# Optimization experiments

Hardware: AMD Instinct MI355X
Metric: run time of the kernel (lower is better)

The kernel has to match this reference:

```python
import jax, jax.numpy as jnp
import numpy as np

D = 128          # embed_dim
T = 500000       # num tokens
N = 100000       # num nodes
EPS = 1e-5       # BatchNorm eps (torch default)


def _mlp(x, g, b, m, v, W1, b1, W2, b2):
    # _GTSMLP in eval mode: BatchNorm1d -> Linear -> ReLU -> Linear (dropouts are identity)
    h = (x - m) * jax.lax.rsqrt(v + EPS) * g + b
    h = jax.nn.relu(h @ W1.T + b1)
    return h @ W2.T + b2


def setup_inputs() -> dict:
    key = jax.random.key(0)
    ks = jax.random.split(key, 12)
    s = 0.02
    return {
        "x": jax.random.normal(ks[0], (T, D), jnp.float32),
        "node_features": jax.random.normal(ks[1], (N, D), jnp.float32),
        "node_batch": jax.random.randint(ks[2], (N,), 0, 8, jnp.int64),
        "token_index": jax.random.randint(ks[3], (2, T), 0, N, jnp.int64),
        # out_proj: BN(D) -> Linear(D, 2D) -> ReLU -> Linear(2D, 2D)
        "op_bn_g": jnp.ones((D,), jnp.float32),
        "op_bn_b": jnp.zeros((D,), jnp.float32),
        "op_bn_m": jnp.zeros((D,), jnp.float32),
        "op_bn_v": jnp.ones((D,), jnp.float32),
        "op_w1": jax.random.normal(ks[4], (2 * D, D), jnp.float32) * s,
        "op_b1": jnp.zeros((2 * D,), jnp.float32),
        "op_w2": jax.random.normal(ks[5], (2 * D, 2 * D), jnp.float32) * s,
        "op_b2": jnp.zeros((2 * D,), jnp.float32),
        # node_mlp: BN(D) -> Linear(D, D) -> ReLU -> Linear(D, D)
        "nm_bn_g": jnp.ones((D,), jnp.float32),
        "nm_bn_b": jnp.zeros((D,), jnp.float32),
        "nm_bn_m": jnp.zeros((D,), jnp.float32),
        "nm_bn_v": jnp.ones((D,), jnp.float32),
        "nm_w1": jax.random.normal(ks[6], (D, D), jnp.float32) * s,
        "nm_b1": jnp.zeros((D,), jnp.float32),
        "nm_w2": jax.random.normal(ks[7], (D, D), jnp.float32) * s,
        "nm_b2": jnp.zeros((D,), jnp.float32),
    }


def reference(x, node_features, node_batch, token_index,
              op_bn_g, op_bn_b, op_bn_m, op_bn_v, op_w1, op_b1, op_w2, op_b2,
              nm_bn_g, nm_bn_b, nm_bn_m, nm_bn_v, nm_w1, nm_b1, nm_w2, nm_b2):
    dim_size = node_batch.shape[0]
    y = _mlp(x, op_bn_g, op_bn_b, op_bn_m, op_bn_v, op_w1, op_b1, op_w2, op_b2)  # [T, 2D]
    # node_features is zeroed in the original; accumulate two scatter-sums
    nf = (jax.ops.segment_sum(y[:, :D], token_index[0], num_segments=dim_size)
          + jax.ops.segment_sum(y[:, D:], token_index[1], num_segments=dim_size))  # [N, D]
    return _mlp(nf, nm_bn_g, nm_bn_b, nm_bn_m, nm_bn_v, nm_w1, nm_b1, nm_w2, nm_b2)
```

## Files before the change

kernel.cpp:

```cpp
#include <hip/hip_runtime.h>
#include <hip/hip_bf16.h>

typedef __bf16 bf16_t;
typedef bf16_t bf16x8 __attribute__((ext_vector_type(8)));
typedef bf16_t bf16x4 __attribute__((ext_vector_type(4)));
typedef bf16_t bf16x2 __attribute__((ext_vector_type(2)));
typedef float  f32x4  __attribute__((ext_vector_type(4)));

#define EPS 1e-5f

__global__ __launch_bounds__(256) void prep_kernel(
    const float* __restrict__ op_w1, const float* __restrict__ op_w2,
    const float* __restrict__ nm_w1, const float* __restrict__ nm_w2,
    const float* __restrict__ op_g, const float* __restrict__ op_b,
    const float* __restrict__ op_m, const float* __restrict__ op_v,
    const float* __restrict__ nm_g, const float* __restrict__ nm_b,
    const float* __restrict__ nm_m, const float* __restrict__ nm_v,
    bf16_t* __restrict__ w1f, bf16_t* __restrict__ w2f,
    bf16_t* __restrict__ nw1f, bf16_t* __restrict__ nw2f,
    float* __restrict__ opsc, float* __restrict__ opsh,
    float* __restrict__ nmsc, float* __restrict__ nmsh)
{
    int t = blockIdx.x * 256 + threadIdx.x;
    if (t < 4096) {
        int g = t, lane = g & 63, nt = (g >> 6) & 15, kt = g >> 10;
        int n = nt * 16 + (lane & 15);
        int k0 = kt * 32 + (lane >> 4) * 8;
        const float* src = op_w1 + (size_t)n * 128 + k0;
        bf16x8 v;
        for (int j = 0; j < 8; ++j) v[j] = (bf16_t)src[j];
        *(bf16x8*)(w1f + (size_t)g * 8) = v;
    } else if (t < 12288) {
        int g = t - 4096, lane = g & 63, nt = (g >> 6) & 15, kt = g >> 10;
        int n = nt * 16 + (lane & 15);
        int k0 = kt * 32 + (lane >> 4) * 8;
        const float* src = op_w2 + (size_t)n * 256 + k0;
        bf16x8 v;
        for (int j = 0; j < 8; ++j) v[j] = (bf16_t)src[j];
        *(bf16x8*)(w2f + (size_t)g * 8) = v;
    } else if (t < 14336) {
        int g = t - 12288, lane = g & 63, nt = (g >> 6) & 7, kt = g >> 9;
        int n = nt * 16 + (lane & 15);
        int k0 = kt * 32 + (lane >> 4) * 8;
        const float* src = nm_w1 + (size_t)n * 128 + k0;
        bf16x8 v;
        for (int j = 0; j < 8; ++j) v[j] = (bf16_t)src[j];
        *(bf16x8*)(nw1f + (size_t)g * 8) = v;
    } else if (t < 16384) {
        int g = t - 14336, lane = g & 63, nt = (g >> 6) & 7, kt = g >> 9;
        int n = nt * 16 + (lane & 15);
        int k0 = kt * 32 + (lane >> 4) * 8;
        const float* src = nm_w2 + (size_t)n * 128 + k0;
        bf16x8 v;
        for (int j = 0; j < 8; ++j) v[j] = (bf16_t)src[j];
        *(bf16x8*)(nw2f + (size_t)g * 8) = v;
    } else if (t < 16512) {
        int c = t - 16384;
        float s = op_g[c] / sqrtf(op_v[c] + EPS);
        opsc[c] = s;
        opsh[c] = op_b[c] - op_m[c] * s;
    } else if (t < 16640) {
        int c = t - 16512;
        float s = nm_g[c] / sqrtf(nm_v[c] + EPS);
        nmsc[c] = s;
        nmsh[c] = nm_b[c] - nm_m[c] * s;
    }
}

__global__ __launch_bounds__(256) void mlp1_y(
    const float* __restrict__ x,
    const float* __restrict__ opsc, const float* __restrict__ opsh,
    const bf16_t* __restrict__ w1f, const bf16_t* __restrict__ w2f,
    const float* __restrict__ b1, const float* __restrict__ b2,
    bf16_t* __restrict__ y, int T)
{
    __shared__ __align__(16) bf16_t Ax[4 * 4 * 64 * 8];
    __shared__ __align__(16) bf16_t Hf[4 * 8 * 64 * 8];
    const int tid  = threadIdx.x;
    const int base = blockIdx.x * 64;

    {
        const int rr = tid >> 4;
        const int kg = tid & 15;
        const int c0 = kg * 8;
        float sc[8], sh[8];
        for (int j = 0; j < 8; ++j) { sc[j] = opsc[c0 + j]; sh[j] = opsh[c0 + j]; }
        for (int p = 0; p < 4; ++p) {
            int r   = p * 16 + rr;
            int tok = base + r;
            float f[8];
            if (tok < T) {
                const float4* xp = (const float4*)(x + (size_t)tok * 128 + c0);
                float4 u = xp[0], w = xp[1];
                f[0] = u.x; f[1] = u.y; f[2] = u.z; f[3] = u.w;
                f[4] = w.x; f[5] = w.y; f[6] = w.z; f[7] = w.w;
            } else {
                for (int j = 0; j < 8; ++j) f[j] = 0.f;
            }
            bf16x8 v;
            for (int j = 0; j < 8; ++j) v[j] = (bf16_t)(f[j] * sc[j] + sh[j]);
            int flat = (((r >> 4) * 4 + (kg >> 2)) * 64 + (kg & 3) * 16 + (r & 15)) * 8;
            *(bf16x8*)(Ax + flat) = v;
        }
    }
    __syncthreads();

    const int w     = tid >> 6;
    const int l     = tid & 63;
    const int colL  = l & 15;
    const int quadw = l >> 4;

    {
        bf16x8 a1[16];
        for (int m = 0; m < 4; ++m)
            for (int kt = 0; kt < 4; ++kt)
                a1[m * 4 + kt] = *(const bf16x8*)(Ax + ((m * 4 + kt) * 64 + l) * 8);
        for (int nt_l = 0; nt_l < 4; ++nt_l) {
            const int nt = nt_l * 4 + w;
            f32x4 acc[4];
            for (int m = 0; m < 4; ++m) acc[m] = (f32x4){0.f, 0.f, 0.f, 0.f};
            for (int kt = 0; kt < 4; ++kt) {
                bf16x8 b = *(const bf16x8*)(w1f + (size_t)((kt * 16 + nt) * 64 + l) * 8);
                for (int m = 0; m < 4; ++m)
                    acc[m] = __builtin_amdgcn_mfma_f32_16x16x32_bf16(a1[m * 4 + kt], b, acc[m], 0, 0, 0);
            }
            float bb = b1[nt * 16 + colL];
            int c   = nt * 16 + colL;
            int kt2 = c >> 5, q2 = (c >> 3) & 3, j2 = c & 7;
            for (int m = 0; m < 4; ++m) {
                int hbase = ((m * 8 + kt2) * 64 + q2 * 16) * 8 + j2;
                for (int reg = 0; reg < 4; ++reg) {
                    float h = acc[m][reg] + bb;
                    h = h > 0.f ? h : 0.f;
                    int m2 = quadw * 4 + reg;
                    Hf[hbase + m2 * 8] = (bf16_t)h;
                }
            }
        }
    }
    __syncthreads();

    for (int mp = 0; mp < 2; ++mp) {
        bf16x8 a2[16];
        for (int mm = 0; mm < 2; ++mm)
            for (int kt = 0; kt < 8; ++kt)
                a2[mm * 8 + kt] = *(const bf16x8*)(Hf + (((2 * mp + mm) * 8 + kt) * 64 + l) * 8);
        for (int nt_l = 0; nt_l < 4; ++nt_l) {
            const int nt = nt_l * 4 + w;
            f32x4 acc0 = {0.f, 0.f, 0.f, 0.f};
            f32x4 acc1 = {0.f, 0.f, 0.f, 0.f};
            for (int kt = 0; kt < 8; ++kt) {
                bf16x8 b = *(const bf16x8*)(w2f + (size_t)((kt * 16 + nt) * 64 + l) * 8);
                acc0 = __builtin_amdgcn_mfma_f32_16x16x32_bf16(a2[kt],     b, acc0, 0, 0, 0);
                acc1 = __builtin_amdgcn_mfma_f32_16x16x32_bf16(a2[8 + kt], b, acc1, 0, 0, 0);
            }
            float bb = b2[nt * 16 + colL];
            int c = nt * 16 + colL;
            for (int reg = 0; reg < 4; ++reg) {
                int r0 = base + (2 * mp) * 16 + quadw * 4 + reg;
                int r1 = base + (2 * mp + 1) * 16 + quadw * 4 + reg;
                if (r0 < T) y[(size_t)r0 * 256 + c] = (bf16_t)(acc0[reg] + bb);
                if (r1 < T) y[(size_t)r1 * 256 + c] = (bf16_t)(acc1[reg] + bb);
            }
        }
    }
}

__global__ __launch_bounds__(256) void count_kernel(
    const int* __restrict__ tix, int* __restrict__ cnt, int T2)
{
    int i = blockIdx.x * 256 + threadIdx.x;
    if (i < T2) atomicAdd(&cnt[tix[i]], 1);
}

__global__ __launch_bounds__(256) void scan1(
    const int* __restrict__ cnt, int* __restrict__ bsum, int N)
{
    __shared__ int lds[256];
    int t = threadIdx.x;
    int i0 = blockIdx.x * 1024 + t * 4;
    int s = 0;
    for (int j = 0; j < 4; ++j) { int i = i0 + j; s += (i < N) ? cnt[i] : 0; }
    lds[t] = s; __syncthreads();
    for (int off = 1; off < 256; off <<= 1) {
        int v = (t >= off) ? lds[t - off] : 0;
        __syncthreads(); lds[t] += v; __syncthreads();
    }
    if (t == 255) bsum[blockIdx.x] = lds[255];
}

__global__ __launch_bounds__(256) void scan2(
    const int* __restrict__ bsum, int* __restrict__ bpref, int nb)
{
    __shared__ int lds[256];
    int t = threadIdx.x;
    int s = (t < nb) ? bsum[t] : 0;
    lds[t] = s; __syncthreads();
    for (int off = 1; off < 256; off <<= 1) {
        int v = (t >= off) ? lds[t - off] : 0;
        __syncthreads(); lds[t] += v; __syncthreads();
    }
    if (t < nb) bpref[t] = lds[t] - s;
}

__global__ __launch_bounds__(256) void scan3(
    const int* __restrict__ cnt, const int* __restrict__ bpref,
    int* __restrict__ offs, int* __restrict__ run, int N)
{
    __shared__ int lds[256];
    int t = threadIdx.x;
    int i0 = blockIdx.x * 1024 + t * 4;
    int c[4]; int s = 0;
    for (int j = 0; j < 4; ++j) { int i = i0 + j; c[j] = (i < N) ? cnt[i] : 0; s += c[j]; }
    lds[t] = s; __syncthreads();
    for (int off = 1; off < 256; off <<= 1) {
        int v = (t >= off) ? lds[t - off] : 0;
        __syncthreads(); lds[t] += v; __syncthreads();
    }
    int p = lds[t] - s + bpref[blockIdx.x];
    for (int j = 0; j < 4; ++j) {
        int i = i0 + j;
        if (i < N) { offs[i] = p; run[i] = p; }
        p += c[j];
    }
}

__global__ __launch_bounds__(256) void fill_kernel(
    const int* __restrict__ tix, int* __restrict__ run,
    int* __restrict__ entries, int T2, int T)
{
    int i = blockIdx.x * 256 + threadIdx.x;
    if (i < T2) {
        int n = tix[i];
        int s = (i >= T) ? 1 : 0;
        int t = s ? (i - T) : i;
        int pos = atomicAdd(&run[n], 1);
        entries[pos] = (t << 1) | s;
    }
}

__global__ __launch_bounds__(256) void gather_mlp2(
    const bf16_t* __restrict__ y,
    const int* __restrict__ offs, const int* __restrict__ cnt,
    const int* __restrict__ entries,
    const float* __restrict__ nmsc, const float* __restrict__ nmsh,
    const bf16_t* __restrict__ w1f, const bf16_t* __restrict__ w2f,
    const float* __restrict__ b1, const float* __restrict__ b2,
    float* __restrict__ out, int N)
{
    __shared__ __align__(16) bf16_t Ax[4 * 4 * 64 * 8];
    __shared__ __align__(16) bf16_t Hf[4 * 4 * 64 * 8];
    const int tid  = threadIdx.x;
    const int base = blockIdx.x * 64;
    const int w    = tid >> 6;
    const int l    = tid & 63;

    {
        const int half = l >> 5;
        const int cl   = l & 31;
        const int c0   = cl * 4;
        float sc[4], sh[4];
        for (int j = 0; j < 4; ++j) { sc[j] = nmsc[c0 + j]; sh[j] = nmsh[c0 + j]; }
        for (int ii = 0; ii < 8; ++ii) {
            int r = w * 16 + ii * 2 + half;
            int n = base + r;
            float a[4] = {0.f, 0.f, 0.f, 0.f};
            if (n < N) {
                int e0 = offs[n], c = cnt[n];
                int e = 0;
                for (; e + 4 <= c; e += 4) {
                    int t0 = entries[e0 + e];
                    int t1 = entries[e0 + e + 1];
                    int t2 = entries[e0 + e + 2];
                    int t3 = entries[e0 + e + 3];
                    bf16x4 v0 = *(const bf16x4*)(y + (size_t)t0 * 128 + c0);
                    bf16x4 v1 = *(const bf16x4*)(y + (size_t)t1 * 128 + c0);
                    bf16x4 v2 = *(const bf16x4*)(y + (size_t)t2 * 128 + c0);
                    bf16x4 v3 = *(const bf16x4*)(y + (size_t)t3 * 128 + c0);
                    for (int j = 0; j < 4; ++j)
                        a[j] += ((float)v0[j] + (float)v1[j]) + ((float)v2[j] + (float)v3[j]);
                }
                for (; e < c; ++e) {
                    int t0 = entries[e0 + e];
                    bf16x4 v0 = *(const bf16x4*)(y + (size_t)t0 * 128 + c0);
                    for (int j = 0; j < 4; ++j) a[j] += (float)v0[j];
                }
            }
            bf16x4 pv;
            for (int j = 0; j < 4; ++j) pv[j] = (bf16_t)(a[j] * sc[j] + sh[j]);
            int idx = ((w * 4 + (c0 >> 5)) * 64 + ((c0 >> 3) & 3) * 16 + (r & 15)) * 8 + (c0 & 7);
            *(bf16x4*)(Ax + idx) = pv;
        }
    }
    __syncthreads();

    const int mt    = w;
    const int colL  = l & 15;
    const int quadw = l >> 4;

    bf16x8 a1f[4];
    for (int kt = 0; kt < 4; ++kt)
        a1f[kt] = *(const bf16x8*)(Ax + ((mt * 4 + kt) * 64 + l) * 8);
    for (int nt = 0; nt < 8; ++nt) {
        f32x4 acc = {0.f, 0.f, 0.f, 0.f};
        for (int kt = 0; kt < 4; ++kt) {
            bf16x8 b = *(const bf16x8*)(w1f + (size_t)((kt * 8 + nt) * 64 + l) * 8);
            acc = __builtin_amdgcn_mfma_f32_16x16x32_bf16(a1f[kt], b, acc, 0, 0, 0);
        }
        float bb = b1[nt * 16 + colL];
        int c   = nt * 16 + colL;
        int kt2 = c >> 5, q2 = (c >> 3) & 3, j2 = c & 7;
        int hbase = ((mt * 4 + kt2) * 64 + q2 * 16) * 8 + j2;
        for (int reg = 0; reg < 4; ++reg) {
            float h = acc[reg] + bb;
            h = h > 0.f ? h : 0.f;
            int m2 = quadw * 4 + reg;
            Hf[hbase + m2 * 8] = (bf16_t)h;
        }
    }

    bf16x8 a2f[4];
    for (int kt = 0; kt < 4; ++kt)
        a2f[kt] = *(const bf16x8*)(Hf + ((mt * 4 + kt) * 64 + l) * 8);
    for (int nt = 0; nt < 8; ++nt) {
        f32x4 acc = {0.f, 0.f, 0.f, 0.f};
        for (int kt = 0; kt < 4; ++kt) {
            bf16x8 b = *(const bf16x8*)(w2f + (size_t)((kt * 8 + nt) * 64 + l) * 8);
            acc = __builtin_amdgcn_mfma_f32_16x16x32_bf16(a2f[kt], b, acc, 0, 0, 0);
        }
        float bb = b2[nt * 16 + colL];
        int c = nt * 16 + colL;
        for (int reg = 0; reg < 4; ++reg) {
            int row = base + mt * 16 + quadw * 4 + reg;
            if (row < N) out[(size_t)row * 128 + c] = acc[reg] + bb;
        }
    }
}

extern "C" void kernel_launch(void* const* d_in, const int* in_sizes, int n_in,
                              void* d_out, int out_size, void* d_ws, size_t ws_size,
                              hipStream_t stream)
{
    const float* x     = (const float*)d_in[0];
    const int*   tix   = (const int*)d_in[3];
    const float* op_g  = (const float*)d_in[4];
    const float* op_b  = (const float*)d_in[5];
    const float* op_m  = (const float*)d_in[6];
    const float* op_v  = (const float*)d_in[7];
    const float* op_w1 = (const float*)d_in[8];
    const float* op_b1 = (const float*)d_in[9];
    const float* op_w2 = (const float*)d_in[10];
    const float* op_b2 = (const float*)d_in[11];
    const float* nm_g  = (const float*)d_in[12];
    const float* nm_b  = (const float*)d_in[13];
    const float* nm_m  = (const float*)d_in[14];
    const float* nm_v  = (const float*)d_in[15];
    const float* nm_w1 = (const float*)d_in[16];
    const float* nm_b1 = (const float*)d_in[17];
    const float* nm_w2 = (const float*)d_in[18];
    const float* nm_b2 = (const float*)d_in[19];

    const int T  = in_sizes[0] / 128;
    const int N  = in_sizes[2];
    const int T2 = 2 * T;

    char* w = (char*)d_ws;
    size_t off = 0;
    bf16_t* y = (bf16_t*)w;              off += (size_t)T * 256 * 2;
    off = (off + 255) & ~(size_t)255;
    bf16_t* w1f  = (bf16_t*)(w + off);   off += (size_t)4096 * 8 * 2;
    bf16_t* w2f  = (bf16_t*)(w + off);   off += (size_t)8192 * 8 * 2;
    bf16_t* nw1f = (bf16_t*)(w + off);   off += (size_t)2048 * 8 * 2;
    bf16_t* nw2f = (bf16_t*)(w + off);   off += (size_t)2048 * 8 * 2;
    float* opsc  = (float*)(w + off);    off += 512;
    float* opsh  = (float*)(w + off);    off += 512;
    float* nmsc  = (float*)(w + off);    off += 512;
    float* nmsh  = (float*)(w + off);    off += 512;
    int* cnt     = (int*)(w + off);      off += (size_t)N * 4;
    int* offs    = (int*)(w + off);      off += (size_t)N * 4;
    int* run     = (int*)(w + off);      off += (size_t)N * 4;
    int* bsum    = (int*)(w + off);      off += 1024 * 4;
    int* bpref   = (int*)(w + off);      off += 1024 * 4;
    int* entries = (int*)(w + off);      off += (size_t)T2 * 4;

    const int nb = (N + 1023) / 1024;

    hipMemsetAsync(cnt, 0, (size_t)N * 4, stream);
    prep_kernel<<<65, 256, 0, stream>>>(op_w1, op_w2, nm_w1, nm_w2,
                                        op_g, op_b, op_m, op_v,
                                        nm_g, nm_b, nm_m, nm_v,
                                        w1f, w2f, nw1f, nw2f,
                                        opsc, opsh, nmsc, nmsh);
    mlp1_y<<<(T + 63) / 64, 256, 0, stream>>>(x, opsc, opsh, w1f, w2f,
                                              op_b1, op_b2, y, T);
    count_kernel<<<(T2 + 255) / 256, 256, 0, stream>>>(tix, cnt, T2);
    scan1<<<nb, 256, 0, stream>>>(cnt, bsum, N);
    scan2<<<1, 256, 0, stream>>>(bsum, bpref, nb);
    scan3<<<nb, 256, 0, stream>>>(cnt, bpref, offs, run, N);
    fill_kernel<<<(T2 + 255) / 256, 256, 0, stream>>>(tix, run, entries, T2, T);
    gather_mlp2<<<(N + 63) / 64, 256, 0, stream>>>(y, offs, cnt, entries,
                                                   nmsc, nmsh, nw1f, nw2f,
                                                   nm_b1, nm_b2, (float*)d_out, N);
}
```

Before: 788.7 us.

## Fold BatchNorm into first-layer weights and fuse index counting into token MLP

Folds the eval-mode BatchNorm scale into the bf16 W1 weights and its shift into a precomputed first-layer bias, for both MLPs. This removes the per-element normalize step in the token and node kernels. Fuses the token-index count atomics into the token MLP kernel, dropping a separate launch. Also makes several local changes: both kernels share one LDS buffer, MFMA operands are swapped so hidden activations are written as 4-wide vectors, launch bounds are set to 4 blocks, and a barrier in the gather kernel is removed. The risks are bf16 rounding differences from scaling the weights and extra atomic contention inside the GEMM kernel.

```diff
diff --git a/kernel.cpp b/kernel.cpp
--- a/kernel.cpp
+++ b/kernel.cpp
@@ -16,10 +16,10 @@
     const float* __restrict__ op_m, const float* __restrict__ op_v,
     const float* __restrict__ nm_g, const float* __restrict__ nm_b,
     const float* __restrict__ nm_m, const float* __restrict__ nm_v,
+    const float* __restrict__ op_b1, const float* __restrict__ nm_b1,
     bf16_t* __restrict__ w1f, bf16_t* __restrict__ w2f,
     bf16_t* __restrict__ nw1f, bf16_t* __restrict__ nw2f,
-    float* __restrict__ opsc, float* __restrict__ opsh,
-    float* __restrict__ nmsc, float* __restrict__ nmsh)
+    float* __restrict__ b1p, float* __restrict__ b1n)
 {
     int t = blockIdx.x * 256 + threadIdx.x;
     if (t < 4096) {
@@ -28,7 +28,11 @@
         int k0 = kt * 32 + (lane >> 4) * 8;
         const float* src = op_w1 + (size_t)n * 128 + k0;
         bf16x8 v;
-        for (int j = 0; j < 8; ++j) v[j] = (bf16_t)src[j];
+        for (int j = 0; j < 8; ++j) {
+            int i = k0 + j;
+            float s = op_g[i] * rsqrtf(op_v[i] + EPS);
+            v[j] = (bf16_t)(src[j] * s);
+        }
         *(bf16x8*)(w1f + (size_t)g * 8) = v;
     } else if (t < 12288) {
         int g = t - 4096, lane = g & 63, nt = (g >> 6) & 15, kt = g >> 10;
@@ -44,7 +48,11 @@
         int k0 = kt * 32 + (lane >> 4) * 8;
         const float* src = nm_w1 + (size_t)n * 128 + k0;
         bf16x8 v;
-        for (int j = 0; j < 8; ++j) v[j] = (bf16_t)src[j];
+        for (int j = 0; j < 8; ++j) {
+            int i = k0 + j;
+            float s = nm_g[i] * rsqrtf(nm_v[i] + EPS);
+            v[j] = (bf16_t)(src[j] * s);
+        }
         *(bf16x8*)(nw1f + (size_t)g * 8) = v;
     } else if (t < 16384) {
         int g = t - 14336, lane = g & 63, nt = (g >> 6) & 7, kt = g >> 9;
@@ -54,37 +62,49 @@
         bf16x8 v;
         for (int j = 0; j < 8; ++j) v[j] = (bf16_t)src[j];
         *(bf16x8*)(nw2f + (size_t)g * 8) = v;
-    } else if (t < 16512) {
-        int c = t - 16384;
-        float s = op_g[c] / sqrtf(op_v[c] + EPS);
-        opsc[c] = s;
-        opsh[c] = op_b[c] - op_m[c] * s;
     } else if (t < 16640) {
-        int c = t - 16512;
-        float s = nm_g[c] / sqrtf(nm_v[c] + EPS);
-        nmsc[c] = s;
-        nmsh[c] = nm_b[c] - nm_m[c] * s;
-    }
-}
-
-__global__ __launch_bounds__(256) void mlp1_y(
+        int o = t - 16384;
+        float acc = op_b1[o];
+        const float* wrow = op_w1 + (size_t)o * 128;
+        for (int i = 0; i < 128; ++i) {
+            float s  = op_g[i] * rsqrtf(op_v[i] + EPS);
+            float sh = op_b[i] - op_m[i] * s;
+            acc += wrow[i] * sh;
+        }
+        b1p[o] = acc;
+    } else if (t < 16768) {
+        int o = t - 16640;
+        float acc = nm_b1[o];
+        const float* wrow = nm_w1 + (size_t)o * 128;
+        for (int i = 0; i < 128; ++i) {
+            float s  = nm_g[i] * rsqrtf(nm_v[i] + EPS);
+            float sh = nm_b[i] - nm_m[i] * s;
+            acc += wrow[i] * sh;
+        }
+        b1n[o] = acc;
+    }
+}
+
+__global__ __launch_bounds__(256, 4) void mlp1_y(
     const float* __restrict__ x,
-    const float* __restrict__ opsc, const float* __restrict__ opsh,
+    const int* __restrict__ tix, int* __restrict__ cnt,
     const bf16_t* __restrict__ w1f, const bf16_t* __restrict__ w2f,
     const float* __restrict__ b1, const float* __restrict__ b2,
-    bf16_t* __restrict__ y, int T)
-{
-    __shared__ __align__(16) bf16_t Ax[4 * 4 * 64 * 8];
-    __shared__ __align__(16) bf16_t Hf[4 * 8 * 64 * 8];
+    bf16_t* __restrict__ y, int T, int T2)
+{
+    __shared__ __align__(16) bf16_t S[4 * 8 * 64 * 8];
     const int tid  = threadIdx.x;
     const int base = blockIdx.x * 64;
+
+    if (tid < 128) {
+        int e = blockIdx.x * 128 + tid;
+        if (e < T2) atomicAdd(&cnt[tix[e]], 1);
+    }
 
     {
         const int rr = tid >> 4;
         const int kg = tid & 15;
         const int c0 = kg * 8;
-        float sc[8], sh[8];
-        for (int j = 0; j < 8; ++j) { sc[j] = opsc[c0 + j]; sh[j] = opsh[c0 + j]; }
         for (int p = 0; p < 4; ++p) {
             int r   = p * 16 + rr;
             int tok = base + r;
@@ -98,9 +118,9 @@
                 for (int j = 0; j < 8; ++j) f[j] = 0.f;
             }
             bf16x8 v;
-            for (int j = 0; j < 8; ++j) v[j] = (bf16_t)(f[j] * sc[j] + sh[j]);
-            int flat = (((r >> 4) * 4 + (kg >> 2)) * 64 + (kg & 3) * 16 + (r & 15)) * 8;
-            *(bf16x8*)(Ax + flat) = v;
+            for (int j = 0; j < 8; ++j) v[j] = (bf16_t)f[j];
+            int flat = ((p * 4 + (kg >> 2)) * 64 + (kg & 3) * 16 + rr) * 8;
+            *(bf16x8*)(S + flat) = v;
         }
     }
     __syncthreads();
@@ -110,32 +130,32 @@
     const int colL  = l & 15;
     const int quadw = l >> 4;
 
-    {
-        bf16x8 a1[16];
-        for (int m = 0; m < 4; ++m)
-            for (int kt = 0; kt < 4; ++kt)
-                a1[m * 4 + kt] = *(const bf16x8*)(Ax + ((m * 4 + kt) * 64 + l) * 8);
-        for (int nt_l = 0; nt_l < 4; ++nt_l) {
-            const int nt = nt_l * 4 + w;
-            f32x4 acc[4];
-            for (int m = 0; m < 4; ++m) acc[m] = (f32x4){0.f, 0.f, 0.f, 0.f};
-            for (int kt = 0; kt < 4; ++kt) {
-                bf16x8 b = *(const bf16x8*)(w1f + (size_t)((kt * 16 + nt) * 64 + l) * 8);
-                for (int m = 0; m < 4; ++m)
-                    acc[m] = __builtin_amdgcn_mfma_f32_16x16x32_bf16(a1[m * 4 + kt], b, acc[m], 0, 0, 0);
+    bf16x8 a1[16];
+    for (int m = 0; m < 4; ++m)
+        for (int kt = 0; kt < 4; ++kt)
+            a1[m * 4 + kt] = *(const bf16x8*)(S + ((m * 4 + kt) * 64 + l) * 8);
+    __syncthreads();
+
+    for (int nt_l = 0; nt_l < 4; ++nt_l) {
+        const int nt = nt_l * 4 + w;
+        f32x4 acc[4];
+        for (int m = 0; m < 4; ++m) acc[m] = (f32x4){0.f, 0.f, 0.f, 0.f};
+        for (int kt = 0; kt < 4; ++kt) {
+            bf16x8 b = *(const bf16x8*)(w1f + (size_t)((kt * 16 + nt) * 64 + l) * 8);
+            for (int m = 0; m < 4; ++m)
+                acc[m] = __builtin_amdgcn_mfma_f32_16x16x32_bf16(b, a1[m * 4 + kt], acc[m], 0, 0, 0);
+        }
+        f32x4 bv = *(const f32x4*)(b1 + nt * 16 + 4 * quadw);
+        const int kt2 = nt >> 1;
+        const int lp  = ((2 * nt + (quadw >> 1)) & 3) * 16 + colL;
+        const int jb  = 4 * (quadw & 1);
+        for (int m = 0; m < 4; ++m) {
+            bf16x4 hv;
+            for (int reg = 0; reg < 4; ++reg) {
+                float h = acc[m][reg] + bv[reg];
+                hv[reg] = (bf16_t)(h > 0.f ? h : 0.f);
             }
-            float bb = b1[nt * 16 + colL];
-            int c   = nt * 16 + colL;
-            int kt2 = c >> 5, q2 = (c >> 3) & 3, j2 = c & 7;
-            for (int m = 0; m < 4; ++m) {
-                int hbase = ((m * 8 + kt2) * 64 + q2 * 16) * 8 + j2;
-                for (int reg = 0; reg < 4; ++reg) {
-                    float h = acc[m][reg] + bb;
-                    h = h > 0.f ? h : 0.f;
-                    int m2 = quadw * 4 + reg;
-                    Hf[hbase + m2 * 8] = (bf16_t)h;
-                }
-            }
+            *(bf16x4*)(S + ((m * 8 + kt2) * 64 + lp) * 8 + jb) = hv;
         }
     }
     __syncthreads();
@@ -144,7 +164,7 @@
         bf16x8 a2[16];
         for (int mm = 0; mm < 2; ++mm)
             for (int kt = 0; kt < 8; ++kt)
-                a2[mm * 8 + kt] = *(const bf16x8*)(Hf + (((2 * mp + mm) * 8 + kt) * 64 + l) * 8);
+                a2[mm * 8 + kt] = *(const bf16x8*)(S + (((2 * mp + mm) * 8 + kt) * 64 + l) * 8);
         for (int nt_l = 0; nt_l < 4; ++nt_l) {
             const int nt = nt_l * 4 + w;
             f32x4 acc0 = {0.f, 0.f, 0.f, 0.f};
@@ -166,13 +186,6 @@
     }
 }
 
-__global__ __launch_bounds__(256) void count_kernel(
-    const int* __restrict__ tix, int* __restrict__ cnt, int T2)
-{
-    int i = blockIdx.x * 256 + threadIdx.x;
-    if (i < T2) atomicAdd(&cnt[tix[i]], 1);
-}
-
 __global__ __launch_bounds__(256) void scan1(
     const int* __restrict__ cnt, int* __restrict__ bsum, int N)
 {
@@ -239,17 +252,15 @@
     }
 }
 
-__global__ __launch_bounds__(256) void gather_mlp2(
+__global__ __launch_bounds__(256, 4) void gather_mlp2(
     const bf16_t* __restrict__ y,
     const int* __restrict__ offs, const int* __restrict__ cnt,
     const int* __restrict__ entries,
-    const float* __restrict__ nmsc, const float* __restrict__ nmsh,
     const bf16_t* __restrict__ w1f, const bf16_t* __restrict__ w2f,
     const float* __restrict__ b1, const float* __restrict__ b2,
     float* __restrict__ out, int N)
 {
-    __shared__ __align__(16) bf16_t Ax[4 * 4 * 64 * 8];
-    __shared__ __align__(16) bf16_t Hf[4 * 4 * 64 * 8];
+    __shared__ __align__(16) bf16_t S[4 * 4 * 64 * 8];
     const int tid  = threadIdx.x;
     const int base = blockIdx.x * 64;
     const int w    = tid >> 6;
@@ -259,8 +270,6 @@
         const int half = l >> 5;
         const int cl   = l & 31;
         const int c0   = cl * 4;
-        float sc[4], sh[4];
-        for (int j = 0; j < 4; ++j) { sc[j] = nmsc[c0 + j]; sh[j] = nmsh[c0 + j]; }
         for (int ii = 0; ii < 8; ++ii) {
             int r = w * 16 + ii * 2 + half;
             int n = base + r;
@@ -287,12 +296,11 @@
                 }
             }
             bf16x4 pv;
-            for (int j = 0; j < 4; ++j) pv[j] = (bf16_t)(a[j] * sc[j] + sh[j]);
+            for (int j = 0; j < 4; ++j) pv[j] = (bf16_t)a[j];
             int idx = ((w * 4 + (c0 >> 5)) * 64 + ((c0 >> 3) & 3) * 16 + (r & 15)) * 8 + (c0 & 7);
-            *(bf16x4*)(Ax + idx) = pv;
-        }
-    }
-    __syncthreads();
+            *(bf16x4*)(S + idx) = pv;
+        }
+    }
 
     const int mt    = w;
     const int colL  = l & 15;
@@ -300,28 +308,29 @@
 
     bf16x8 a1f[4];
     for (int kt = 0; kt < 4; ++kt)
-        a1f[kt] = *(const bf16x8*)(Ax + ((mt * 4 + kt) * 64 + l) * 8);
+        a1f[kt] = *(const bf16x8*)(S + ((mt * 4 + kt) * 64 + l) * 8);
+
     for (int nt = 0; nt < 8; ++nt) {
         f32x4 acc = {0.f, 0.f, 0.f, 0.f};
         for (int kt = 0; kt < 4; ++kt) {
             bf16x8 b = *(const bf16x8*)(w1f + (size_t)((kt * 8 + nt) * 64 + l) * 8);
-            acc = __builtin_amdgcn_mfma_f32_16x16x32_bf16(a1f[kt], b, acc, 0, 0, 0);
-        }
-        float bb = b1[nt * 16 + colL];
-        int c   = nt * 16 + colL;
-        int kt2 = c >> 5, q2 = (c >> 3) & 3, j2 = c & 7;
-        int hbase = ((mt * 4 + kt2) * 64 + q2 * 16) * 8 + j2;
+            acc = __builtin_amdgcn_mfma_f32_16x16x32_bf16(b, a1f[kt], acc, 0, 0, 0);
+        }
+        f32x4 bv = *(const f32x4*)(b1 + nt * 16 + 4 * quadw);
+        const int kt2 = nt >> 1;
+        const int lp  = ((2 * nt + (quadw >> 1)) & 3) * 16 + colL;
+        const int jb  = 4 * (quadw & 1);
+        bf16x4 hv;
         for (int reg = 0; reg < 4; ++reg) {
-            float h = acc[reg] + bb;
-            h = h > 0.f ? h : 0.f;
-            int m2 = quadw * 4 + reg;
-            Hf[hbase + m2 * 8] = (bf16_t)h;
-        }
+            float h = acc[reg] + bv[reg];
+            hv[reg] = (bf16_t)(h > 0.f ? h : 0.f);
+        }
+        *(bf16x4*)(S + ((mt * 4 + kt2) * 64 + lp) * 8 + jb) = hv;
     }
 
     bf16x8 a2f[4];
     for (int kt = 0; kt < 4; ++kt)
-        a2f[kt] = *(const bf16x8*)(Hf + ((mt * 4 + kt) * 64 + l) * 8);
+        a2f[kt] = *(const bf16x8*)(S + ((mt * 4 + kt) * 64 + l) * 8);
     for (int nt = 0; nt < 8; ++nt) {
         f32x4 acc = {0.f, 0.f, 0.f, 0.f};
         for (int kt = 0; kt < 4; ++kt) {
@@ -372,10 +381,8 @@
     bf16_t* w2f  = (bf16_t*)(w + off);   off += (size_t)8192 * 8 * 2;
     bf16_t* nw1f = (bf16_t*)(w + off);   off += (size_t)2048 * 8 * 2;
     bf16_t* nw2f = (bf16_t*)(w + off);   off += (size_t)2048 * 8 * 2;
-    float* opsc  = (float*)(w + off);    off += 512;
-    float* opsh  = (float*)(w + off);    off += 512;
-    float* nmsc  = (float*)(w + off);    off += 512;
-    float* nmsh  = (float*)(w + off);    off += 512;
+    float* b1p   = (float*)(w + off);    off += 256 * 4;
+    float* b1n   = (float*)(w + off);    off += 128 * 4;
     int* cnt     = (int*)(w + off);      off += (size_t)N * 4;
     int* offs    = (int*)(w + off);      off += (size_t)N * 4;
     int* run     = (int*)(w + off);      off += (size_t)N * 4;
@@ -386,19 +393,18 @@
     const int nb = (N + 1023) / 1024;
 
     hipMemsetAsync(cnt, 0, (size_t)N * 4, stream);
-    prep_kernel<<<65, 256, 0, stream>>>(op_w1, op_w2, nm_w1, nm_w2,
+    prep_kernel<<<66, 256, 0, stream>>>(op_w1, op_w2, nm_w1, nm_w2,
                                         op_g, op_b, op_m, op_v,
                                         nm_g, nm_b, nm_m, nm_v,
-                                        w1f, w2f, nw1f, nw2f,
-                                        opsc, opsh, nmsc, nmsh);
-    mlp1_y<<<(T + 63) / 64, 256, 0, stream>>>(x, opsc, opsh, w1f, w2f,
-                                              op_b1, op_b2, y, T);
-    count_kernel<<<(T2 + 255) / 256, 256, 0, stream>>>(tix, cnt, T2);
+                                        op_b1, nm_b1,
+                                        w1f, w2f, nw1f, nw2f, b1p, b1n);
+    mlp1_y<<<(T + 63) / 64, 256, 0, stream>>>(x, tix, cnt, w1f, w2f,
+                                              b1p, op_b2, y, T, T2);
     scan1<<<nb, 256, 0, stream>>>(cnt, bsum, N);
     scan2<<<1, 256, 0, stream>>>(bsum, bpref, nb);
     scan3<<<nb, 256, 0, stream>>>(cnt, bpref, offs, run, N);
     fill_kernel<<<(T2 + 255) / 256, 256, 0, stream>>>(tix, run, entries, T2, T);
     gather_mlp2<<<(N + 63) / 64, 256, 0, stream>>>(y, offs, cnt, entries,
-                                                   nmsc, nmsh, nw1f, nw2f,
-                                                   nm_b1, nm_b2, (float*)d_out, N);
-}
+                                                   nw1f, nw2f,
+                                                   b1n, nm_b2, (float*)d_out, N);
+}
```

Result: slower. 994.1 us (+26.0%).
